# Kernel tuning notes

Measured on AMD Instinct MI355X. Metric: run time of the kernel, lower is better.

Reference implementation:

```python
import jax, jax.numpy as jnp
import numpy as np

B, S, C = 8, 2048, 512

def setup_inputs() -> dict:
    key = jax.random.key(0)
    ks = jax.random.split(key, 7)
    s = 1.0 / np.sqrt(C)
    return {
        "x": jax.random.normal(ks[0], (B, S, C), dtype=jnp.float32),
        "Wq": jax.random.uniform(ks[1], (C, C), jnp.float32, -s, s),
        "bq": jax.random.uniform(ks[2], (C,), jnp.float32, -s, s),
        "Wk": jax.random.uniform(ks[3], (C, C), jnp.float32, -s, s),
        "bk": jax.random.uniform(ks[4], (C,), jnp.float32, -s, s),
        "Wv": jax.random.uniform(ks[5], (C, C), jnp.float32, -s, s),
        "bv": jax.random.uniform(ks[6], (C,), jnp.float32, -s, s),
    }

def reference(x, Wq, bq, Wk, bk, Wv, bv):
    # Linear projections (torch Linear: x @ W.T + b)
    q = jnp.einsum('bsc,dc->bsd', x, Wq) + bq
    k = jnp.einsum('bsc,dc->bsd', x, Wk) + bk
    v = jnp.einsum('bsc,dc->bsd', x, Wv) + bv
    # NOTE: original code computes dk but never scales by 1/sqrt(dk)
    scores = jnp.einsum('bqd,bkd->bqk', q, k)          # [B,S,S]
    attn = jax.nn.softmax(scores, axis=-1)
    out = jnp.einsum('bqk,bkd->bqd', attn, v)
    return out + x
```

## Files before the change

### kernel.cpp

```cpp
#include <hip/hip_runtime.h>
#include <hip/hip_bf16.h>


typedef __bf16 bf16_t;
typedef bf16_t bf16x8 __attribute__((ext_vector_type(8)));
typedef float floatx4 __attribute__((ext_vector_type(4)));

#define MFMA16(a, b, c) __builtin_amdgcn_mfma_f32_16x16x32_bf16((a), (b), (c), 0, 0, 0)
#define FLASH_LDS 141824

__device__ __forceinline__ void gload16(const void* g, void* l) {
    __builtin_amdgcn_global_load_lds((const __attribute__((address_space(1))) void*)g,
                                     (__attribute__((address_space(3))) void*)l, 16, 0, 0);
}

__device__ __forceinline__ float wave16_sum(float v) {
    v += __shfl_xor(v, 1);
    v += __shfl_xor(v, 2);
    v += __shfl_xor(v, 4);
    v += __shfl_xor(v, 8);
    return v;
}

__global__ void convert_in(const float* __restrict__ X,
                           const float* __restrict__ Wq, const float* __restrict__ Wk,
                           const float* __restrict__ Wv, const float* __restrict__ bq,
                           const float* __restrict__ bk, const float* __restrict__ bv,
                           bf16_t* __restrict__ Xb, bf16_t* __restrict__ Wb,
                           float* __restrict__ biasc) {
    int bid = blockIdx.x, tid = threadIdx.x;
    if (bid < 4096) {
        size_t e0 = ((size_t)bid * 256 + tid) * 8;
        float4 f0 = *(const float4*)(X + e0);
        float4 f1 = *(const float4*)(X + e0 + 4);
        bf16x8 o;
        o[0] = (bf16_t)f0.x; o[1] = (bf16_t)f0.y; o[2] = (bf16_t)f0.z; o[3] = (bf16_t)f0.w;
        o[4] = (bf16_t)f1.x; o[5] = (bf16_t)f1.y; o[6] = (bf16_t)f1.z; o[7] = (bf16_t)f1.w;
        *(bf16x8*)(Xb + e0) = o;
    } else {
        int idx = (bid - 4096) * 256 + tid;
        int e0 = idx * 4;
        int row = e0 >> 9, c = e0 & 511;
        const float* src;
        if (row < 512)       src = Wq + row * 512;
        else if (row < 1024) src = Wk + (row - 512) * 512;
        else                 src = Wv + (row - 1024) * 512;
        float4 v = *(const float4*)(src + c);
        Wb[e0 + 0] = (bf16_t)v.x;
        Wb[e0 + 1] = (bf16_t)v.y;
        Wb[e0 + 2] = (bf16_t)v.z;
        Wb[e0 + 3] = (bf16_t)v.w;
        if (idx < 1536) {
            float b;
            if (idx < 512)       b = bq[idx];
            else if (idx < 1024) b = bk[idx - 512];
            else                 b = bv[idx - 1024];
            biasc[idx] = b;
        }
    }
}

__global__ __launch_bounds__(256, 2)
void qkv_gemm(const bf16_t* __restrict__ Xb, const bf16_t* __restrict__ Wb,
              const float* __restrict__ biasc, bf16_t* __restrict__ Q,
              bf16_t* __restrict__ K, bf16_t* __restrict__ Vt) {
    __shared__ int4 smem4[2560];
    char* As = (char*)smem4;
    char* Bs = (char*)smem4 + 16384;
    char* Vtile = (char*)smem4;

    const int tid = threadIdx.x;
    const int l = tid & 63, w = tid >> 6;
    const int lane16 = l & 15, lq = l >> 4;
    const int klo = lane16 & 7;
    const int m0 = (blockIdx.x & 127) << 7;
    const int n0 = (blockIdx.x >> 7) << 7;
    const int wm = (w >> 1) << 6, wn = (w & 1) << 6;
    const int srow = l >> 3;
    const int sc8 = (l & 7) ^ srow;

    floatx4 acc[4][4];
#pragma unroll
    for (int a = 0; a < 4; ++a)
#pragma unroll
        for (int bb = 0; bb < 4; ++bb) acc[a][bb] = (floatx4){0.f, 0.f, 0.f, 0.f};

    for (int it = 0; it < 8; ++it) {
        __syncthreads();
#pragma unroll
        for (int j = 0; j < 4; ++j) {
            int seg = j * 4 + w;
            int row = seg * 8 + srow;
            gload16(Xb + (size_t)(m0 + row) * 512 + it * 64 + sc8 * 8, As + seg * 1024);
            gload16(Wb + (size_t)(n0 + row) * 512 + it * 64 + sc8 * 8, Bs + seg * 1024);
        }
        __syncthreads();
#pragma unroll
        for (int kst = 0; kst < 2; ++kst) {
            bf16x8 afr[4], bfr[4];
#pragma unroll
            for (int mt = 0; mt < 4; ++mt)
                afr[mt] = *(const bf16x8*)(As + (wm + mt * 16 + lane16) * 128 +
                                           ((kst * 4 + lq) ^ klo) * 16);
#pragma unroll
            for (int nt = 0; nt < 4; ++nt)
                bfr[nt] = *(const bf16x8*)(Bs + (wn + nt * 16 + lane16) * 128 +
                                           ((kst * 4 + lq) ^ klo) * 16);
#pragma unroll
            for (int mt = 0; mt < 4; ++mt)
#pragma unroll
                for (int nt = 0; nt < 4; ++nt)
                    acc[mt][nt] = MFMA16(afr[mt], bfr[nt], acc[mt][nt]);
        }
    }

    float bias_v[4];
#pragma unroll
    for (int nt = 0; nt < 4; ++nt) bias_v[nt] = biasc[n0 + wn + nt * 16 + lane16];

    if (n0 < 1024) {
        bf16_t* Dst = (n0 < 512) ? Q : K;
        const int coff = (n0 < 512 ? n0 : n0 - 512) + wn;
#pragma unroll
        for (int mt = 0; mt < 4; ++mt)
#pragma unroll
            for (int nt = 0; nt < 4; ++nt)
#pragma unroll
                for (int i = 0; i < 4; ++i) {
                    int rowM = m0 + wm + mt * 16 + lq * 4 + i;
                    Dst[(size_t)rowM * 512 + coff + nt * 16 + lane16] =
                        (bf16_t)(acc[mt][nt][i] + bias_v[nt]);
                }
    } else {
        __syncthreads();
#pragma unroll
        for (int mt = 0; mt < 4; ++mt)
#pragma unroll
            for (int nt = 0; nt < 4; ++nt)
#pragma unroll
                for (int i = 0; i < 4; ++i) {
                    int dl = wn + nt * 16 + lane16;
                    int sl = wm + mt * 16 + lq * 4 + i;
                    *(bf16_t*)(Vtile + dl * 264 + sl * 2) =
                        (bf16_t)(acc[mt][nt][i] + bias_v[nt]);
                }
        __syncthreads();
        const int bb = m0 >> 11, s0 = m0 & 2047, dbase = n0 - 1024;
#pragma unroll
        for (int j = 0; j < 8; ++j) {
            int slot = j * 256 + tid;
            int dd = slot >> 4, c = slot & 15;
            *(int4*)(Vt + (size_t)(bb * 512 + dbase + dd) * 2048 + s0 + c * 8) =
                *(const int4*)(Vtile + dd * 264 + c * 16);
        }
    }
}

__global__ __launch_bounds__(512, 2)
void flash_attn_v8(const bf16_t* __restrict__ Q, const bf16_t* __restrict__ K,
                   const bf16_t* __restrict__ Vt, const float* __restrict__ X,
                   float* __restrict__ Out) {
    extern __shared__ char smem[];
    float* lpart = (float*)(smem + 141312);

    const int tid = threadIdx.x;
    const int l = tid & 63, w = tid >> 6;
    const int lane16 = l & 15, lq = l >> 4;
    const int qg = w >> 1, h = w & 1;
    const int dbase = w << 6;
    const int b = blockIdx.x & 7;
    const int q0 = (blockIdx.x >> 3) << 6;

    const bf16_t* Kbase = K + (size_t)b * 2048 * 512;
    const bf16_t* Vbase = Vt + (size_t)b * 512 * 2048;

    const int dl_v = ((l >> 3) << 1) | ((l & 7) >> 2);
    const int vc   = (l & 3) ^ ((l >> 3) & 3);

    auto stageK = [&](int kt, char* Kb) {
#pragma unroll
        for (int j = 0; j < 4; ++j) {
            int seg = j * 8 + w;
            int c = (l & ~7) | ((l & 7) ^ (seg & 7));
            gload16(Kbase + ((size_t)kt * 32 + seg) * 512 + c * 8, Kb + seg * 1024);
        }
    };
    auto stageV = [&](int kt, char* Vb) {
        const bf16_t* Vsrc = Vbase + kt * 32;
#pragma unroll
        for (int j = 0; j < 4; ++j) {
            int seg = j * 8 + w;
            int d = seg * 16 + dl_v;
            gload16(Vsrc + (size_t)d * 2048 + vc * 8, Vb + seg * 1024);
        }
    };

    stageK(0, smem);
    stageV(0, smem + 65536);

    bf16x8 qf[16];
    const bf16_t* Qrow = Q + (size_t)(b * 2048 + q0 + qg * 16 + lane16) * 512 + lq * 8;
#pragma unroll
    for (int kst = 0; kst < 16; ++kst) qf[kst] = *(const bf16x8*)(Qrow + kst * 32);

    floatx4 o[16];
#pragma unroll
    for (int t = 0; t < 16; ++t) o[t] = (floatx4){0.f, 0.f, 0.f, 0.f};
    float lsum[4] = {0.f, 0.f, 0.f, 0.f};
    const float L2E = 1.4426950408889634f;
    const int key = h * 16 + lane16;
    const int prow = qg * 16 + lq * 4;

    __syncthreads();

    stageK(1, smem + 32768);
    {
        floatx4 sc = (floatx4){0.f, 0.f, 0.f, 0.f};
#pragma unroll
        for (int kst = 0; kst < 16; ++kst) {
            int i0 = kst * 4 + lq;
            int p0 = (i0 & ~7) | ((i0 & 7) ^ (key & 7));
            bf16x8 kb = *(const bf16x8*)(smem + key * 1024 + p0 * 16);
            sc = MFMA16(qf[kst], kb, sc);
        }
#pragma unroll
        for (int i = 0; i < 4; ++i) {
            float p = __builtin_exp2f(sc[i] * L2E);
            lsum[i] += p;
            *(bf16_t*)(smem + 131072 + (prow + i) * 80 + key * 2) = (bf16_t)p;
        }
    }
    __syncthreads();

    for (int kt = 0; kt < 64; ++kt) {
        char* Knext = smem + ((kt + 1) & 1) * 32768;
        char* Vcur  = smem + 65536 + (kt & 1) * 32768;
        char* Pcur  = smem + 131072 + (kt & 1) * 5120;
        char* Pnext = smem + 131072 + ((kt + 1) & 1) * 5120;

        if (kt < 62) stageK(kt + 2, smem + (kt & 1) * 32768);
        if (kt < 63) stageV(kt + 1, smem + 65536 + ((kt + 1) & 1) * 32768);

        floatx4 sc = (floatx4){0.f, 0.f, 0.f, 0.f};
        if (kt < 63) {
#pragma unroll
            for (int kst = 0; kst < 16; ++kst) {
                int i0 = kst * 4 + lq;
                int p0 = (i0 & ~7) | ((i0 & 7) ^ (key & 7));
                bf16x8 kb = *(const bf16x8*)(Knext + key * 1024 + p0 * 16);
                sc = MFMA16(qf[kst], kb, sc);
            }
        }

        {
            bf16x8 pa[4], vb[4];
#pragma unroll
            for (int qgi = 0; qgi < 4; ++qgi)
                pa[qgi] = *(const bf16x8*)(Pcur + (qgi * 16 + lane16) * 80 + lq * 16);
#pragma unroll
            for (int dg = 0; dg < 4; ++dg) {
                int d = dbase + dg * 16 + lane16;
                int slot = (d & 1) * 4 + (lq ^ ((d >> 1) & 3));
                vb[dg] = *(const bf16x8*)(Vcur + (d >> 1) * 128 + slot * 16);
            }
#pragma unroll
            for (int dg = 0; dg < 4; ++dg)
#pragma unroll
                for (int qgi = 0; qgi < 4; ++qgi)
                    o[qgi * 4 + dg] = MFMA16(pa[qgi], vb[dg], o[qgi * 4 + dg]);
        }

        if (kt < 63) {
#pragma unroll
            for (int i = 0; i < 4; ++i) {
                float p = __builtin_exp2f(sc[i] * L2E);
                lsum[i] += p;
                *(bf16_t*)(Pnext + (prow + i) * 80 + key * 2) = (bf16_t)p;
            }
        }

        __syncthreads();
    }

#pragma unroll
    for (int i = 0; i < 4; ++i) {
        float s = wave16_sum(lsum[i]);
        if (lane16 == 0) lpart[(prow + i) * 2 + h] = s;
    }
    __syncthreads();

#pragma unroll
    for (int qgi = 0; qgi < 4; ++qgi) {
        float rinv[4];
#pragma unroll
        for (int i = 0; i < 4; ++i) {
            int row = qgi * 16 + lq * 4 + i;
            rinv[i] = 1.0f / (lpart[row * 2] + lpart[row * 2 + 1]);
        }
#pragma unroll
        for (int dg = 0; dg < 4; ++dg) {
            int d = dbase + dg * 16 + lane16;
#pragma unroll
            for (int i = 0; i < 4; ++i) {
                int row = q0 + qgi * 16 + lq * 4 + i;
                size_t g = (size_t)(b * 2048 + row) * 512 + d;
                Out[g] = o[qgi * 4 + dg][i] * rinv[i] + X[g];
            }
        }
    }
}

extern "C" void kernel_launch(void* const* d_in, const int* in_sizes, int n_in,
                              void* d_out, int out_size, void* d_ws, size_t ws_size,
                              hipStream_t stream) {
    const float* x  = (const float*)d_in[0];
    const float* Wq = (const float*)d_in[1];
    const float* bq = (const float*)d_in[2];
    const float* Wk = (const float*)d_in[3];
    const float* bk = (const float*)d_in[4];
    const float* Wv = (const float*)d_in[5];
    const float* bv = (const float*)d_in[6];
    float* out = (float*)d_out;
    char* ws = (char*)d_ws;

    bf16_t* Wb    = (bf16_t*)(ws);
    float*  biasc = (float*)(ws + 1572864);
    bf16_t* Xb    = (bf16_t*)(ws + 1579008);
    bf16_t* Qb    = (bf16_t*)(ws + 18356224);
    bf16_t* Kb    = (bf16_t*)(ws + 35133440);
    bf16_t* Vt    = (bf16_t*)(ws + 51910656);

    convert_in<<<4864, 256, 0, stream>>>(x, Wq, Wk, Wv, bq, bk, bv, Xb, Wb, biasc);
    qkv_gemm<<<1536, 256, 0, stream>>>(Xb, Wb, biasc, Qb, Kb, Vt);

    hipFuncSetAttribute(reinterpret_cast<const void*>(flash_attn_v8),
                        hipFuncAttributeMaxDynamicSharedMemorySize, FLASH_LDS);
    flash_attn_v8<<<256, 512, FLASH_LDS, stream>>>(Qb, Kb, Vt, x, out);
}
```

Measured before the change: 228.6 us.

## Split flash attention waves into QK producer and PV consumer roles

Waves are specialized. Four producer waves each compute the full 32-key score tile for 16 query rows, apply exp and write P to LDS. Four consumer waves each handle 128 output dims across all 64 query rows, doing the PV MFMAs. This is meant to let QK/softmax and PV work run on separate waves and to drop the cross-wave row-sum combine. The consumer waves now hold 32 accumulator tiles, which raises register pressure, and the work per wave becomes unbalanced between the two roles.

```diff
diff --git a/kernel.cpp b/kernel.cpp
--- a/kernel.cpp
+++ b/kernel.cpp
@@ -7,7 +7,7 @@
 typedef float floatx4 __attribute__((ext_vector_type(4)));
 
 #define MFMA16(a, b, c) __builtin_amdgcn_mfma_f32_16x16x32_bf16((a), (b), (c), 0, 0, 0)
-#define FLASH_LDS 141824
+#define FLASH_LDS 141568
 
 __device__ __forceinline__ void gload16(const void* g, void* l) {
     __builtin_amdgcn_global_load_lds((const __attribute__((address_space(1))) void*)g,
@@ -157,7 +157,7 @@
 }
 
 __global__ __launch_bounds__(512, 2)
-void flash_attn_v8(const bf16_t* __restrict__ Q, const bf16_t* __restrict__ K,
+void flash_attn_v9(const bf16_t* __restrict__ Q, const bf16_t* __restrict__ K,
                    const bf16_t* __restrict__ Vt, const float* __restrict__ X,
                    float* __restrict__ Out) {
     extern __shared__ char smem[];
@@ -166,8 +166,8 @@
     const int tid = threadIdx.x;
     const int l = tid & 63, w = tid >> 6;
     const int lane16 = l & 15, lq = l >> 4;
-    const int qg = w >> 1, h = w & 1;
-    const int dbase = w << 6;
+    const bool producer = (w < 4);
+    const int dbase = (w - 4) << 7;
     const int b = blockIdx.x & 7;
     const int q0 = (blockIdx.x >> 3) << 6;
 
@@ -199,35 +199,43 @@
     stageV(0, smem + 65536);
 
     bf16x8 qf[16];
-    const bf16_t* Qrow = Q + (size_t)(b * 2048 + q0 + qg * 16 + lane16) * 512 + lq * 8;
-#pragma unroll
-    for (int kst = 0; kst < 16; ++kst) qf[kst] = *(const bf16x8*)(Qrow + kst * 32);
-
-    floatx4 o[16];
-#pragma unroll
-    for (int t = 0; t < 16; ++t) o[t] = (floatx4){0.f, 0.f, 0.f, 0.f};
+    if (producer) {
+        const bf16_t* Qrow = Q + (size_t)(b * 2048 + q0 + w * 16 + lane16) * 512 + lq * 8;
+#pragma unroll
+        for (int kst = 0; kst < 16; ++kst) qf[kst] = *(const bf16x8*)(Qrow + kst * 32);
+    }
     float lsum[4] = {0.f, 0.f, 0.f, 0.f};
     const float L2E = 1.4426950408889634f;
-    const int key = h * 16 + lane16;
-    const int prow = qg * 16 + lq * 4;
+    const int prow = w * 16 + lq * 4;
+
+    floatx4 o[32];
+#pragma unroll
+    for (int t = 0; t < 32; ++t) o[t] = (floatx4){0.f, 0.f, 0.f, 0.f};
 
     __syncthreads();
 
     stageK(1, smem + 32768);
-    {
-        floatx4 sc = (floatx4){0.f, 0.f, 0.f, 0.f};
+    if (producer) {
+        floatx4 sc0 = (floatx4){0.f, 0.f, 0.f, 0.f};
+        floatx4 sc1 = (floatx4){0.f, 0.f, 0.f, 0.f};
 #pragma unroll
         for (int kst = 0; kst < 16; ++kst) {
             int i0 = kst * 4 + lq;
-            int p0 = (i0 & ~7) | ((i0 & 7) ^ (key & 7));
-            bf16x8 kb = *(const bf16x8*)(smem + key * 1024 + p0 * 16);
-            sc = MFMA16(qf[kst], kb, sc);
+            int k0 = lane16, k1 = 16 + lane16;
+            int p0 = (i0 & ~7) | ((i0 & 7) ^ (k0 & 7));
+            int p1 = (i0 & ~7) | ((i0 & 7) ^ (k1 & 7));
+            bf16x8 kb0 = *(const bf16x8*)(smem + k0 * 1024 + p0 * 16);
+            bf16x8 kb1 = *(const bf16x8*)(smem + k1 * 1024 + p1 * 16);
+            sc0 = MFMA16(qf[kst], kb0, sc0);
+            sc1 = MFMA16(qf[kst], kb1, sc1);
         }
 #pragma unroll
         for (int i = 0; i < 4; ++i) {
-            float p = __builtin_exp2f(sc[i] * L2E);
-            lsum[i] += p;
-            *(bf16_t*)(smem + 131072 + (prow + i) * 80 + key * 2) = (bf16_t)p;
+            float pa = __builtin_exp2f(sc0[i] * L2E);
+            float pb = __builtin_exp2f(sc1[i] * L2E);
+            lsum[i] += pa + pb;
+            *(bf16_t*)(smem + 131072 + (prow + i) * 80 + lane16 * 2) = (bf16_t)pa;
+            *(bf16_t*)(smem + 131072 + (prow + i) * 80 + 32 + lane16 * 2) = (bf16_t)pb;
         }
     }
     __syncthreads();
@@ -241,70 +249,74 @@
         if (kt < 62) stageK(kt + 2, smem + (kt & 1) * 32768);
         if (kt < 63) stageV(kt + 1, smem + 65536 + ((kt + 1) & 1) * 32768);
 
-        floatx4 sc = (floatx4){0.f, 0.f, 0.f, 0.f};
-        if (kt < 63) {
-#pragma unroll
-            for (int kst = 0; kst < 16; ++kst) {
-                int i0 = kst * 4 + lq;
-                int p0 = (i0 & ~7) | ((i0 & 7) ^ (key & 7));
-                bf16x8 kb = *(const bf16x8*)(Knext + key * 1024 + p0 * 16);
-                sc = MFMA16(qf[kst], kb, sc);
+        if (producer) {
+            if (kt < 63) {
+                floatx4 sc0 = (floatx4){0.f, 0.f, 0.f, 0.f};
+                floatx4 sc1 = (floatx4){0.f, 0.f, 0.f, 0.f};
+#pragma unroll
+                for (int kst = 0; kst < 16; ++kst) {
+                    int i0 = kst * 4 + lq;
+                    int k0 = lane16, k1 = 16 + lane16;
+                    int p0 = (i0 & ~7) | ((i0 & 7) ^ (k0 & 7));
+                    int p1 = (i0 & ~7) | ((i0 & 7) ^ (k1 & 7));
+                    bf16x8 kb0 = *(const bf16x8*)(Knext + k0 * 1024 + p0 * 16);
+                    bf16x8 kb1 = *(const bf16x8*)(Knext + k1 * 1024 + p1 * 16);
+                    sc0 = MFMA16(qf[kst], kb0, sc0);
+                    sc1 = MFMA16(qf[kst], kb1, sc1);
+                }
+#pragma unroll
+                for (int i = 0; i < 4; ++i) {
+                    float pa = __builtin_exp2f(sc0[i] * L2E);
+                    float pb = __builtin_exp2f(sc1[i] * L2E);
+                    lsum[i] += pa + pb;
+                    *(bf16_t*)(Pnext + (prow + i) * 80 + lane16 * 2) = (bf16_t)pa;
+                    *(bf16_t*)(Pnext + (prow + i) * 80 + 32 + lane16 * 2) = (bf16_t)pb;
+                }
             }
-        }
-
-        {
-            bf16x8 pa[4], vb[4];
-#pragma unroll
-            for (int qgi = 0; qgi < 4; ++qgi)
-                pa[qgi] = *(const bf16x8*)(Pcur + (qgi * 16 + lane16) * 80 + lq * 16);
-#pragma unroll
-            for (int dg = 0; dg < 4; ++dg) {
+        } else {
+            bf16x8 pa[4];
+#pragma unroll
+            for (int qh = 0; qh < 4; ++qh)
+                pa[qh] = *(const bf16x8*)(Pcur + (qh * 16 + lane16) * 80 + lq * 16);
+#pragma unroll
+            for (int dg = 0; dg < 8; ++dg) {
                 int d = dbase + dg * 16 + lane16;
                 int slot = (d & 1) * 4 + (lq ^ ((d >> 1) & 3));
-                vb[dg] = *(const bf16x8*)(Vcur + (d >> 1) * 128 + slot * 16);
+                bf16x8 vb = *(const bf16x8*)(Vcur + (d >> 1) * 128 + slot * 16);
+#pragma unroll
+                for (int qh = 0; qh < 4; ++qh)
+                    o[qh * 8 + dg] = MFMA16(pa[qh], vb, o[qh * 8 + dg]);
             }
-#pragma unroll
-            for (int dg = 0; dg < 4; ++dg)
-#pragma unroll
-                for (int qgi = 0; qgi < 4; ++qgi)
-                    o[qgi * 4 + dg] = MFMA16(pa[qgi], vb[dg], o[qgi * 4 + dg]);
-        }
-
-        if (kt < 63) {
-#pragma unroll
-            for (int i = 0; i < 4; ++i) {
-                float p = __builtin_exp2f(sc[i] * L2E);
-                lsum[i] += p;
-                *(bf16_t*)(Pnext + (prow + i) * 80 + key * 2) = (bf16_t)p;
-            }
-        }
-
-        __syncthreads();
-    }
-
-#pragma unroll
-    for (int i = 0; i < 4; ++i) {
-        float s = wave16_sum(lsum[i]);
-        if (lane16 == 0) lpart[(prow + i) * 2 + h] = s;
+        }
+
+        __syncthreads();
+    }
+
+    if (producer) {
+#pragma unroll
+        for (int i = 0; i < 4; ++i) {
+            float s = wave16_sum(lsum[i]);
+            if (lane16 == 0) lpart[prow + i] = s;
+        }
     }
     __syncthreads();
 
-#pragma unroll
-    for (int qgi = 0; qgi < 4; ++qgi) {
-        float rinv[4];
-#pragma unroll
-        for (int i = 0; i < 4; ++i) {
-            int row = qgi * 16 + lq * 4 + i;
-            rinv[i] = 1.0f / (lpart[row * 2] + lpart[row * 2 + 1]);
-        }
-#pragma unroll
-        for (int dg = 0; dg < 4; ++dg) {
-            int d = dbase + dg * 16 + lane16;
-#pragma unroll
-            for (int i = 0; i < 4; ++i) {
-                int row = q0 + qgi * 16 + lq * 4 + i;
-                size_t g = (size_t)(b * 2048 + row) * 512 + d;
-                Out[g] = o[qgi * 4 + dg][i] * rinv[i] + X[g];
+    if (!producer) {
+#pragma unroll
+        for (int qh = 0; qh < 4; ++qh) {
+            float rinv[4];
+#pragma unroll
+            for (int i = 0; i < 4; ++i)
+                rinv[i] = 1.0f / lpart[qh * 16 + lq * 4 + i];
+#pragma unroll
+            for (int dg = 0; dg < 8; ++dg) {
+                int d = dbase + dg * 16 + lane16;
+#pragma unroll
+                for (int i = 0; i < 4; ++i) {
+                    int row = q0 + qh * 16 + lq * 4 + i;
+                    size_t g = (size_t)(b * 2048 + row) * 512 + d;
+                    Out[g] = o[qh * 8 + dg][i] * rinv[i] + X[g];
+                }
             }
         }
     }
@@ -333,7 +345,7 @@
     convert_in<<<4864, 256, 0, stream>>>(x, Wq, Wk, Wv, bq, bk, bv, Xb, Wb, biasc);
     qkv_gemm<<<1536, 256, 0, stream>>>(Xb, Wb, biasc, Qb, Kb, Vt);
 
-    hipFuncSetAttribute(reinterpret_cast<const void*>(flash_attn_v8),
+    hipFuncSetAttribute(reinterpret_cast<const void*>(flash_attn_v9),
                         hipFuncAttributeMaxDynamicSharedMemorySize, FLASH_LDS);
-    flash_attn_v8<<<256, 512, FLASH_LDS, stream>>>(Qb, Kb, Vt, x, out);
-}
+    flash_attn_v9<<<256, 512, FLASH_LDS, stream>>>(Qb, Kb, Vt, x, out);
+}
```

New measurement: 250.0 us. 1.09x slower.
